# Optimization experiments

Measured on AMD Instinct MI355X. Metric: run time of the kernel, lower is better.

Reference implementation:

```python
import jax, jax.numpy as jnp
import numpy as np
import math

EMBED, HEADS, LEVELS, POINTS = 256, 8, 4, 4
HEAD_DIM = EMBED // HEADS


def _init_offset_bias():
    # replicates MSDeformableAttention._reset_parameters grid init for sampling_offsets.bias
    thetas = np.arange(HEADS, dtype=np.float32) * (2.0 * math.pi / HEADS)
    grid = np.stack([np.cos(thetas), np.sin(thetas)], -1)
    grid = grid / np.abs(grid).max(-1, keepdims=True)
    grid = np.tile(grid.reshape(HEADS, 1, 1, 2), (1, LEVELS, POINTS, 1))
    grid = grid * np.arange(1, POINTS + 1, dtype=np.float32).reshape(1, 1, -1, 1)
    return jnp.asarray(grid.reshape(-1))


def setup_inputs():
    key = jax.random.key(0)
    ks = jax.random.split(key, 8)
    bs, Lq = 4, 900
    shapes = np.array([[100, 100], [50, 50], [25, 25], [13, 13]], dtype=np.int32)
    areas = shapes[:, 0] * shapes[:, 1]
    Lv = int(areas.sum())  # 13294
    start = np.concatenate([[0], np.cumsum(areas)[:-1]]).astype(np.int32)
    s = 0.02
    return {
        'query': jax.random.normal(ks[0], (bs, Lq, EMBED), jnp.float32),
        'reference_points': jax.random.uniform(ks[1], (bs, Lq, LEVELS, 2), jnp.float32),
        'value': jax.random.normal(ks[2], (bs, Lv, EMBED), jnp.float32),
        'value_spatial_shapes': jnp.asarray(shapes),
        'value_level_start_index': jnp.asarray(start),
        'w_value': jax.random.normal(ks[3], (EMBED, EMBED), jnp.float32) * s,
        'b_value': jnp.zeros((EMBED,), jnp.float32),
        'w_offsets': jax.random.normal(ks[4], (HEADS * LEVELS * POINTS * 2, EMBED), jnp.float32) * s,
        'b_offsets': _init_offset_bias(),
        'w_attn': jax.random.normal(ks[5], (HEADS * LEVELS * POINTS, EMBED), jnp.float32) * s,
        'b_attn': jnp.zeros((HEADS * LEVELS * POINTS,), jnp.float32),
        'w_out': jax.random.normal(ks[6], (EMBED, EMBED), jnp.float32) * s,
        'b_out': jnp.zeros((EMBED,), jnp.float32),
    }


def _ms_deform_attn(value, spatial_shapes, start_index, loc, attn):
    # value: [bs, Lv, H, D]; loc: [bs, Lq, H, L, P, 2] normalized in [0,1]; attn: [bs, Lq, H, L, P]
    bs, Lv, nh, hd = value.shape
    Lq = loc.shape[1]
    v = value.transpose(0, 2, 1, 3)  # [bs, H, Lv, D]
    Wf = spatial_shapes[:, 1].astype(loc.dtype).reshape(1, 1, 1, LEVELS, 1)
    Hf = spatial_shapes[:, 0].astype(loc.dtype).reshape(1, 1, 1, LEVELS, 1)
    Wi = spatial_shapes[:, 1].reshape(1, 1, 1, LEVELS, 1)
    Hi = spatial_shapes[:, 0].reshape(1, 1, 1, LEVELS, 1)
    start = start_index.reshape(1, 1, 1, LEVELS, 1)
    # grid_sample(align_corners=False, padding_mode='zeros'): pixel coord = loc * size - 0.5
    x = loc[..., 0] * Wf - 0.5
    y = loc[..., 1] * Hf - 0.5
    x0 = jnp.floor(x)
    y0 = jnp.floor(y)
    lx = x - x0
    ly = y - y0
    x0i = x0.astype(jnp.int32)
    y0i = y0.astype(jnp.int32)

    def corner(xi, yi, w):
        valid = (xi >= 0) & (xi < Wi) & (yi >= 0) & (yi < Hi)
        idx = start + jnp.clip(yi, 0, Hi - 1) * Wi + jnp.clip(xi, 0, Wi - 1)  # global flat index into Lv
        idx = idx.transpose(0, 2, 1, 3, 4).reshape(bs, nh, Lq * LEVELS * POINTS)
        g = jnp.take_along_axis(v, idx[..., None], axis=2)  # [bs, H, Lq*L*P, D]
        g = g.reshape(bs, nh, Lq, LEVELS, POINTS, hd)
        w = (w * valid.astype(loc.dtype)).transpose(0, 2, 1, 3, 4)  # [bs, H, Lq, L, P]
        return g * w[..., None]

    sampled = (corner(x0i, y0i, (1 - lx) * (1 - ly))
               + corner(x0i + 1, y0i, lx * (1 - ly))
               + corner(x0i, y0i + 1, (1 - lx) * ly)
               + corner(x0i + 1, y0i + 1, lx * ly))  # [bs, H, Lq, L, P, D]
    aw = attn.transpose(0, 2, 1, 3, 4)  # [bs, H, Lq, L, P]
    out = (sampled * aw[..., None]).sum(axis=(3, 4))  # [bs, H, Lq, D]
    return out.transpose(0, 2, 1, 3).reshape(bs, Lq, nh * hd)


def reference(query, reference_points, value, value_spatial_shapes, value_level_start_index, w_value, b_value, w_offsets, b_offsets, w_attn, b_attn, w_out, b_out):
    bs, Lq, _ = query.shape
    Lv = value.shape[1]
    v = (value @ w_value.T + b_value).reshape(bs, Lv, HEADS, HEAD_DIM)
    off = (query @ w_offsets.T + b_offsets).reshape(bs, Lq, HEADS, LEVELS, POINTS, 2)
    attn = jax.nn.softmax((query @ w_attn.T + b_attn).reshape(bs, Lq, HEADS, LEVELS * POINTS), axis=-1)
    attn = attn.reshape(bs, Lq, HEADS, LEVELS, POINTS)
    # offset_normalizer = spatial_shapes.flip(1) -> (W, H) per level
    norm = value_spatial_shapes[:, ::-1].astype(query.dtype).reshape(1, 1, 1, LEVELS, 1, 2)
    loc = reference_points[:, :, None, :, None, :] + off / norm  # [bs, Lq, H, L, P, 2]
    out = _ms_deform_attn(v, value_spatial_shapes, value_level_start_index, loc, attn)
    return out @ w_out.T + b_out
```

## Files before the change

kernel.cpp:

```cpp
#include <hip/hip_runtime.h>
#include <cstddef>

#define EMBED 256
#define HEADS 8
#define LEVELS 4
#define POINTS 4
#define NQOUT 384

typedef __attribute__((ext_vector_type(8))) short bf16x8;
typedef __attribute__((ext_vector_type(4))) float f32x4;

__device__ __forceinline__ unsigned short bf16_rn(float x) {
    union { float f; unsigned u; } v; v.f = x;
    const unsigned r = v.u + 0x7fffu + ((v.u >> 16) & 1u);
    return (unsigned short)(r >> 16);
}
__device__ __forceinline__ float bf16_to_f(unsigned short h) {
    union { unsigned u; float f; } v; v.u = (unsigned)h << 16;
    return v.f;
}

__global__ __launch_bounds__(256) void gemm_mfma_split(
    const float* __restrict__ A, const float* __restrict__ B,
    const float* __restrict__ bias, float* __restrict__ C, int M)
{
    __shared__ unsigned short AsH[128 * 32], AsL[128 * 32];
    __shared__ unsigned short BsH[128 * 32], BsL[128 * 32];

    const int tid  = threadIdx.x;
    const int lane = tid & 63;
    const int wid  = tid >> 6;
    const int wm   = (wid >> 1) * 64;
    const int wn   = (wid & 1) * 64;
    const int m0   = blockIdx.y * 128;
    const int n0   = blockIdx.x * 128;

    const int sr = tid >> 1;
    const int sc = (tid & 1) * 16;

    const bool mok = (m0 + sr) < M;
    const float* ga = A + (size_t)(m0 + sr) * 256 + sc;
    const float* gb = B + (size_t)(n0 + sr) * 256 + sc;

    f32x4 acc[4][4] = {};

    for (int k0 = 0; k0 < 256; k0 += 32) {
        #pragma unroll
        for (int i = 0; i < 4; ++i) {
            const int byte_in_row = (sc + i * 4) * 2;
            int addr = sr * 64 + byte_in_row;
            addr ^= (sr & 7) << 4;

            float4 va = make_float4(0.f, 0.f, 0.f, 0.f);
            if (mok) va = *(const float4*)(ga + k0 + i * 4);
            const unsigned short ah0 = bf16_rn(va.x), ah1 = bf16_rn(va.y);
            const unsigned short ah2 = bf16_rn(va.z), ah3 = bf16_rn(va.w);
            const unsigned short al0 = bf16_rn(va.x - bf16_to_f(ah0));
            const unsigned short al1 = bf16_rn(va.y - bf16_to_f(ah1));
            const unsigned short al2 = bf16_rn(va.z - bf16_to_f(ah2));
            const unsigned short al3 = bf16_rn(va.w - bf16_to_f(ah3));
            *(uint2*)((char*)AsH + addr) =
                make_uint2((unsigned)ah0 | ((unsigned)ah1 << 16),
                           (unsigned)ah2 | ((unsigned)ah3 << 16));
            *(uint2*)((char*)AsL + addr) =
                make_uint2((unsigned)al0 | ((unsigned)al1 << 16),
                           (unsigned)al2 | ((unsigned)al3 << 16));

            const float4 vb = *(const float4*)(gb + k0 + i * 4);
            const unsigned short bh0 = bf16_rn(vb.x), bh1 = bf16_rn(vb.y);
            const unsigned short bh2 = bf16_rn(vb.z), bh3 = bf16_rn(vb.w);
            const unsigned short bl0 = bf16_rn(vb.x - bf16_to_f(bh0));
            const unsigned short bl1 = bf16_rn(vb.y - bf16_to_f(bh1));
            const unsigned short bl2 = bf16_rn(vb.z - bf16_to_f(bh2));
            const unsigned short bl3 = bf16_rn(vb.w - bf16_to_f(bh3));
            *(uint2*)((char*)BsH + addr) =
                make_uint2((unsigned)bh0 | ((unsigned)bh1 << 16),
                           (unsigned)bh2 | ((unsigned)bh3 << 16));
            *(uint2*)((char*)BsL + addr) =
                make_uint2((unsigned)bl0 | ((unsigned)bl1 << 16),
                           (unsigned)bl2 | ((unsigned)bl3 << 16));
        }
        __syncthreads();

        bf16x8 ah[4], al[4], bh[4], bl[4];
        const int kb = (lane >> 4) * 16;
        #pragma unroll
        for (int f = 0; f < 4; ++f) {
            const int rowA = wm + f * 16 + (lane & 15);
            int aaddr = rowA * 64 + kb;  aaddr ^= (rowA & 7) << 4;
            ah[f] = *(const bf16x8*)((const char*)AsH + aaddr);
            al[f] = *(const bf16x8*)((const char*)AsL + aaddr);
            const int rowB = wn + f * 16 + (lane & 15);
            int baddr = rowB * 64 + kb;  baddr ^= (rowB & 7) << 4;
            bh[f] = *(const bf16x8*)((const char*)BsH + baddr);
            bl[f] = *(const bf16x8*)((const char*)BsL + baddr);
        }
        #pragma unroll
        for (int mi = 0; mi < 4; ++mi)
            #pragma unroll
            for (int ni = 0; ni < 4; ++ni) {
                acc[mi][ni] = __builtin_amdgcn_mfma_f32_16x16x32_bf16(
                    ah[mi], bh[ni], acc[mi][ni], 0, 0, 0);
                acc[mi][ni] = __builtin_amdgcn_mfma_f32_16x16x32_bf16(
                    ah[mi], bl[ni], acc[mi][ni], 0, 0, 0);
                acc[mi][ni] = __builtin_amdgcn_mfma_f32_16x16x32_bf16(
                    al[mi], bh[ni], acc[mi][ni], 0, 0, 0);
            }
        __syncthreads();
    }

    #pragma unroll
    for (int mi = 0; mi < 4; ++mi) {
        #pragma unroll
        for (int j = 0; j < 4; ++j) {
            const int m = m0 + wm + mi * 16 + ((lane >> 4) << 2) + j;
            if (m >= M) continue;
            #pragma unroll
            for (int ni = 0; ni < 4; ++ni) {
                const int n = n0 + wn + ni * 16 + (lane & 15);
                C[(size_t)m * 256 + n] = acc[mi][ni][j] + bias[n];
            }
        }
    }
}

template<int TM, int TN, int TK>
__global__ __launch_bounds__(256) void gemm_abt_bias(
    const float* __restrict__ A, const float* __restrict__ B,
    const float* __restrict__ bias, float* __restrict__ C,
    int M, int N, int K)
{
    __shared__ float As[TK][TM + 4];
    __shared__ float Bs[TK][TN + 4];
    const int tid = threadIdx.x;
    const int m0 = blockIdx.y * TM;
    const int n0 = blockIdx.x * TN;
    const int tx = tid & 15;
    const int ty = tid >> 4;
    const int ar  = tid >> 2;
    const int ac4 = (tid & 3) << 2;

    float acc[4][4] = {};

    for (int k0 = 0; k0 < K; k0 += TK) {
        {
            const int m = m0 + ar;
            float4 va = make_float4(0.f, 0.f, 0.f, 0.f);
            if (m < M) va = *(const float4*)(A + (size_t)m * K + k0 + ac4);
            As[ac4 + 0][ar] = va.x; As[ac4 + 1][ar] = va.y;
            As[ac4 + 2][ar] = va.z; As[ac4 + 3][ar] = va.w;

            const int n = n0 + ar;
            const float4 vb = *(const float4*)(B + (size_t)n * K + k0 + ac4);
            Bs[ac4 + 0][ar] = vb.x; Bs[ac4 + 1][ar] = vb.y;
            Bs[ac4 + 2][ar] = vb.z; Bs[ac4 + 3][ar] = vb.w;
        }
        __syncthreads();

        #pragma unroll
        for (int k = 0; k < TK; ++k) {
            const float4 a4 = *(const float4*)(&As[k][ty << 2]);
            const float4 b4 = *(const float4*)(&Bs[k][tx << 2]);
            const float a[4] = {a4.x, a4.y, a4.z, a4.w};
            const float b[4] = {b4.x, b4.y, b4.z, b4.w};
            #pragma unroll
            for (int i = 0; i < 4; ++i)
                #pragma unroll
                for (int j = 0; j < 4; ++j)
                    acc[i][j] = fmaf(a[i], b[j], acc[i][j]);
        }
        __syncthreads();
    }

    #pragma unroll
    for (int i = 0; i < 4; ++i) {
        const int m = m0 + (ty << 2) + i;
        if (m >= M) continue;
        #pragma unroll
        for (int j = 0; j < 4; ++j) {
            const int n = n0 + (tx << 2) + j;
            C[(size_t)m * N + n] = acc[i][j] + bias[n];
        }
    }
}

__global__ __launch_bounds__(256) void gemm_query_fused(
    const float* __restrict__ A,
    const float* __restrict__ Boff,  const float* __restrict__ Battn,
    const float* __restrict__ boff,  const float* __restrict__ battn,
    float* __restrict__ C, int M, int K)
{
    constexpr int TM = 64, TN = 64, TK = 16;
    __shared__ float As[TK][TM + 4];
    __shared__ float Bs[TK][TN + 4];
    const int tid = threadIdx.x;
    const int m0 = blockIdx.y * TM;
    const int n0 = blockIdx.x * TN;
    const bool isAttn = (n0 >= 256);
    const float* __restrict__ B  = isAttn ? Battn : Boff;
    const float* __restrict__ bv = isAttn ? battn : boff;
    const int nbase = isAttn ? (n0 - 256) : n0;

    const int tx = tid & 15;
    const int ty = tid >> 4;
    const int ar  = tid >> 2;
    const int ac4 = (tid & 3) << 2;

    float acc[4][4] = {};

    for (int k0 = 0; k0 < K; k0 += TK) {
        {
            const int m = m0 + ar;
            float4 va = make_float4(0.f, 0.f, 0.f, 0.f);
            if (m < M) va = *(const float4*)(A + (size_t)m * K + k0 + ac4);
            As[ac4 + 0][ar] = va.x; As[ac4 + 1][ar] = va.y;
            As[ac4 + 2][ar] = va.z; As[ac4 + 3][ar] = va.w;

            const float4 vb = *(const float4*)(B + (size_t)(nbase + ar) * K + k0 + ac4);
            Bs[ac4 + 0][ar] = vb.x; Bs[ac4 + 1][ar] = vb.y;
            Bs[ac4 + 2][ar] = vb.z; Bs[ac4 + 3][ar] = vb.w;
        }
        __syncthreads();

        #pragma unroll
        for (int k = 0; k < TK; ++k) {
            const float4 a4 = *(const float4*)(&As[k][ty << 2]);
            const float4 b4 = *(const float4*)(&Bs[k][tx << 2]);
            const float a[4] = {a4.x, a4.y, a4.z, a4.w};
            const float b[4] = {b4.x, b4.y, b4.z, b4.w};
            #pragma unroll
            for (int i = 0; i < 4; ++i)
                #pragma unroll
                for (int j = 0; j < 4; ++j)
                    acc[i][j] = fmaf(a[i], b[j], acc[i][j]);
        }
        __syncthreads();
    }

    #pragma unroll
    for (int i = 0; i < 4; ++i) {
        const int m = m0 + (ty << 2) + i;
        if (m >= M) continue;
        #pragma unroll
        for (int j = 0; j < 4; ++j) {
            const int nl = (tx << 2) + j;
            C[(size_t)m * NQOUT + n0 + nl] = acc[i][j] + bv[nbase + nl];
        }
    }
}

__global__ __launch_bounds__(256) void ms_sample_kernel(
    const float* __restrict__ vproj,
    const float* __restrict__ refp,
    const float* __restrict__ qout,
    const int*   __restrict__ shapes,
    const int*   __restrict__ startix,
    float* __restrict__ sampled,
    int Lq, int Lv)
{
    __shared__ float aw_lds[HEADS * LEVELS * POINTS];

    const int bq = blockIdx.x;
    const int b  = bq / Lq;
    const int tid = threadIdx.x;
    const int h = tid >> 5, d = tid & 31;

    const float* vb   = vproj + (size_t)b * Lv * EMBED;
    const float* rowq = qout + (size_t)bq * NQOUT;
    const float* offq = rowq;
    const float* logq = rowq + 256;
    const float* refq = refp + (size_t)bq * LEVELS * 2;

    if (tid < HEADS * LEVELS * POINTS) {
        const float v = logq[tid];
        float m = v;
        #pragma unroll
        for (int s = 8; s > 0; s >>= 1) m = fmaxf(m, __shfl_xor(m, s, 16));
        const float e = __expf(v - m);
        float sum = e;
        #pragma unroll
        for (int s = 8; s > 0; s >>= 1) sum += __shfl_xor(sum, s, 16);
        aw_lds[tid] = e / sum;
    }
    __syncthreads();

    float accv = 0.f;
    #pragma unroll
    for (int l = 0; l < LEVELS; ++l) {
        const int H = shapes[l * 2 + 0];
        const int W = shapes[l * 2 + 1];
        const int st = startix[l];
        const float fW = (float)W, fH = (float)H;
        const float rx = refq[l * 2 + 0];
        const float ry = refq[l * 2 + 1];
        #pragma unroll
        for (int p = 0; p < POINTS; ++p) {
            const int oi = (((h * LEVELS + l) * POINTS) + p) * 2;
            const float ox = offq[oi + 0];
            const float oy = offq[oi + 1];
            const float aw = aw_lds[(h * LEVELS + l) * POINTS + p];
            const float x = (rx + ox / fW) * fW - 0.5f;
            const float y = (ry + oy / fH) * fH - 0.5f;
            const float x0f = floorf(x), y0f = floorf(y);
            const float lx = x - x0f, ly = y - y0f;
            const int x0 = (int)x0f, y0 = (int)y0f;
            float s = 0.f;
            #pragma unroll
            for (int c = 0; c < 4; ++c) {
                const int xi = x0 + (c & 1);
                const int yi = y0 + (c >> 1);
                const float wx = (c & 1) ? lx : 1.f - lx;
                const float wy = (c >> 1) ? ly : 1.f - ly;
                const bool valid = (xi >= 0) && (xi < W) && (yi >= 0) && (yi < H);
                const int xc = min(max(xi, 0), W - 1);
                const int yc = min(max(yi, 0), H - 1);
                const float val = vb[(size_t)(st + yc * W + xc) * EMBED + (h << 5) + d];
                s = fmaf(valid ? wx * wy : 0.f, val, s);
            }
            accv = fmaf(aw, s, accv);
        }
    }
    sampled[(size_t)bq * EMBED + tid] = accv;
}

extern "C" void kernel_launch(void* const* d_in, const int* in_sizes, int n_in,
                              void* d_out, int out_size, void* d_ws, size_t ws_size,
                              hipStream_t stream)
{
    const float* query   = (const float*)d_in[0];
    const float* refp    = (const float*)d_in[1];
    const float* value   = (const float*)d_in[2];
    const int*   shapes  = (const int*)d_in[3];
    const int*   startix = (const int*)d_in[4];
    const float* w_value = (const float*)d_in[5];
    const float* b_value = (const float*)d_in[6];
    const float* w_off   = (const float*)d_in[7];
    const float* b_off   = (const float*)d_in[8];
    const float* w_attn  = (const float*)d_in[9];
    const float* b_attn  = (const float*)d_in[10];
    const float* w_out   = (const float*)d_in[11];
    const float* b_out   = (const float*)d_in[12];
    float* out = (float*)d_out;

    const int bs = 4;
    const int Lq = in_sizes[0] / (bs * EMBED);
    const int Lv = in_sizes[2] / (bs * EMBED);
    const int BQ = bs * Lq;

    float* ws = (float*)d_ws;
    float* vproj   = ws; ws += (size_t)bs * Lv * EMBED;
    float* qoutb   = ws; ws += (size_t)BQ * NQOUT;
    float* sampled = ws; ws += (size_t)BQ * EMBED;

    {
        const int M = bs * Lv;
        dim3 grid(EMBED / 128, (M + 127) / 128);
        hipLaunchKernelGGL(gemm_mfma_split, grid, dim3(256), 0, stream,
                           value, w_value, b_value, vproj, M);
    }
    {
        dim3 grid(NQOUT / 64, (BQ + 63) / 64);
        hipLaunchKernelGGL(gemm_query_fused, grid, dim3(256), 0, stream,
                           query, w_off, w_attn, b_off, b_attn, qoutb, BQ, EMBED);
    }
    {
        hipLaunchKernelGGL(ms_sample_kernel, dim3(BQ), dim3(256), 0, stream,
                           vproj, refp, qoutb, shapes, startix, sampled, Lq, Lv);
    }
    {
        dim3 grid(EMBED / 64, (BQ + 63) / 64);
        hipLaunchKernelGGL((gemm_abt_bias<64, 64, 16>), grid, dim3(256), 0, stream,
                           sampled, w_out, b_out, out, BQ, EMBED, EMBED);
    }
}
```

Baseline: 226.1 us.

## Pre-split value weight into swizzled bf16 hi/lo once and DMA into LDS

Adds a prep kernel that converts w_value into pre-swizzled bf16 hi/lo halves once per call, so the value projection no longer redoes that conversion in every tile. The projection kernel now tiles 64 rows by the full 256 columns, so the A tile is converted only once per row block instead of once per column tile. Weight tiles are loaded straight into LDS with global_load_lds. This costs an extra kernel launch and a larger LDS footprint for B, and there is no double buffering.

Result: no change. 221.7 us (-2.0%).

```diff
diff --git a/kernel.cpp b/kernel.cpp
--- a/kernel.cpp
+++ b/kernel.cpp
@@ -19,66 +19,94 @@
     union { unsigned u; float f; } v; v.u = (unsigned)h << 16;
     return v.f;
 }
-
-__global__ __launch_bounds__(256) void gemm_mfma_split(
-    const float* __restrict__ A, const float* __restrict__ B,
+__device__ __forceinline__ int sw_addr(int row, int byte_in_row) {
+    return (row * 64 + byte_in_row) ^ ((row & 7) << 4);
+}
+
+__global__ __launch_bounds__(256) void prep_w(
+    const float* __restrict__ w,
+    unsigned short* __restrict__ hi, unsigned short* __restrict__ lo)
+{
+    const int t  = blockIdx.x * 256 + threadIdx.x;
+    const int r  = t >> 3;
+    const int kp = t & 7;
+    const float* src = w + (size_t)r * 256 + kp * 32;
+    #pragma unroll
+    for (int c = 0; c < 4; ++c) {
+        unsigned hw[4], lw[4];
+        #pragma unroll
+        for (int j = 0; j < 4; ++j) {
+            const float f0 = src[c * 8 + j * 2 + 0];
+            const float f1 = src[c * 8 + j * 2 + 1];
+            const unsigned short h0 = bf16_rn(f0), h1 = bf16_rn(f1);
+            const unsigned short l0 = bf16_rn(f0 - bf16_to_f(h0));
+            const unsigned short l1 = bf16_rn(f1 - bf16_to_f(h1));
+            hw[j] = (unsigned)h0 | ((unsigned)h1 << 16);
+            lw[j] = (unsigned)l0 | ((unsigned)l1 << 16);
+        }
+        const int addr = kp * 16384 + sw_addr(r, c * 16);
+        *(uint4*)((char*)hi + addr) = make_uint4(hw[0], hw[1], hw[2], hw[3]);
+        *(uint4*)((char*)lo + addr) = make_uint4(lw[0], lw[1], lw[2], lw[3]);
+    }
+}
+
+__global__ __launch_bounds__(256) void vproj_mfma(
+    const float* __restrict__ A,
+    const unsigned short* __restrict__ Bhi, const unsigned short* __restrict__ Blo,
     const float* __restrict__ bias, float* __restrict__ C, int M)
 {
-    __shared__ unsigned short AsH[128 * 32], AsL[128 * 32];
-    __shared__ unsigned short BsH[128 * 32], BsL[128 * 32];
+    __shared__ unsigned short AsH[64 * 32], AsL[64 * 32];
+    __shared__ unsigned short BsH[256 * 32], BsL[256 * 32];
 
     const int tid  = threadIdx.x;
     const int lane = tid & 63;
-    const int wid  = tid >> 6;
-    const int wm   = (wid >> 1) * 64;
-    const int wn   = (wid & 1) * 64;
-    const int m0   = blockIdx.y * 128;
-    const int n0   = blockIdx.x * 128;
-
-    const int sr = tid >> 1;
-    const int sc = (tid & 1) * 16;
-
+    const int wn   = (tid >> 6) * 64;
+    const int m0   = blockIdx.x * 64;
+
+    const int sr = tid >> 2;
+    const int sc = (tid & 3) * 8;
     const bool mok = (m0 + sr) < M;
     const float* ga = A + (size_t)(m0 + sr) * 256 + sc;
-    const float* gb = B + (size_t)(n0 + sr) * 256 + sc;
+
+    const int wbase = (tid & 192) * 16;
 
     f32x4 acc[4][4] = {};
 
-    for (int k0 = 0; k0 < 256; k0 += 32) {
+    for (int kp = 0; kp < 8; ++kp) {
         #pragma unroll
         for (int i = 0; i < 4; ++i) {
-            const int byte_in_row = (sc + i * 4) * 2;
-            int addr = sr * 64 + byte_in_row;
-            addr ^= (sr & 7) << 4;
-
+            const int off = i * 4096 + wbase + (lane << 4);
+            __builtin_amdgcn_global_load_lds(
+                (const __attribute__((address_space(1))) unsigned int*)
+                    ((const char*)Bhi + kp * 16384 + off),
+                (__attribute__((address_space(3))) unsigned int*)
+                    ((char*)BsH + i * 4096 + wbase),
+                16, 0, 0);
+            __builtin_amdgcn_global_load_lds(
+                (const __attribute__((address_space(1))) unsigned int*)
+                    ((const char*)Blo + kp * 16384 + off),
+                (__attribute__((address_space(3))) unsigned int*)
+                    ((char*)BsL + i * 4096 + wbase),
+                16, 0, 0);
+        }
+
+        #pragma unroll
+        for (int q = 0; q < 2; ++q) {
             float4 va = make_float4(0.f, 0.f, 0.f, 0.f);
-            if (mok) va = *(const float4*)(ga + k0 + i * 4);
-            const unsigned short ah0 = bf16_rn(va.x), ah1 = bf16_rn(va.y);
-            const unsigned short ah2 = bf16_rn(va.z), ah3 = bf16_rn(va.w);
-            const unsigned short al0 = bf16_rn(va.x - bf16_to_f(ah0));
-            const unsigned short al1 = bf16_rn(va.y - bf16_to_f(ah1));
-            const unsigned short al2 = bf16_rn(va.z - bf16_to_f(ah2));
-            const unsigned short al3 = bf16_rn(va.w - bf16_to_f(ah3));
+            if (mok) va = *(const float4*)(ga + kp * 32 + q * 4);
+            const unsigned short h0 = bf16_rn(va.x), h1 = bf16_rn(va.y);
+            const unsigned short h2 = bf16_rn(va.z), h3 = bf16_rn(va.w);
+            const unsigned short l0 = bf16_rn(va.x - bf16_to_f(h0));
+            const unsigned short l1 = bf16_rn(va.y - bf16_to_f(h1));
+            const unsigned short l2 = bf16_rn(va.z - bf16_to_f(h2));
+            const unsigned short l3 = bf16_rn(va.w - bf16_to_f(h3));
+            const int addr = sw_addr(sr, (sc + q * 4) * 2);
             *(uint2*)((char*)AsH + addr) =
-                make_uint2((unsigned)ah0 | ((unsigned)ah1 << 16),
-                           (unsigned)ah2 | ((unsigned)ah3 << 16));
+                make_uint2((unsigned)h0 | ((unsigned)h1 << 16),
+                           (unsigned)h2 | ((unsigned)h3 << 16));
             *(uint2*)((char*)AsL + addr) =
-                make_uint2((unsigned)al0 | ((unsigned)al1 << 16),
-                           (unsigned)al2 | ((unsigned)al3 << 16));
-
-            const float4 vb = *(const float4*)(gb + k0 + i * 4);
-            const unsigned short bh0 = bf16_rn(vb.x), bh1 = bf16_rn(vb.y);
-            const unsigned short bh2 = bf16_rn(vb.z), bh3 = bf16_rn(vb.w);
-            const unsigned short bl0 = bf16_rn(vb.x - bf16_to_f(bh0));
-            const unsigned short bl1 = bf16_rn(vb.y - bf16_to_f(bh1));
-            const unsigned short bl2 = bf16_rn(vb.z - bf16_to_f(bh2));
-            const unsigned short bl3 = bf16_rn(vb.w - bf16_to_f(bh3));
-            *(uint2*)((char*)BsH + addr) =
-                make_uint2((unsigned)bh0 | ((unsigned)bh1 << 16),
-                           (unsigned)bh2 | ((unsigned)bh3 << 16));
-            *(uint2*)((char*)BsL + addr) =
-                make_uint2((unsigned)bl0 | ((unsigned)bl1 << 16),
-                           (unsigned)bl2 | ((unsigned)bl3 << 16));
+                make_uint2((unsigned)l0 | ((unsigned)l1 << 16),
+                           (unsigned)l2 | ((unsigned)l3 << 16));
         }
         __syncthreads();
 
@@ -86,12 +114,10 @@
         const int kb = (lane >> 4) * 16;
         #pragma unroll
         for (int f = 0; f < 4; ++f) {
-            const int rowA = wm + f * 16 + (lane & 15);
-            int aaddr = rowA * 64 + kb;  aaddr ^= (rowA & 7) << 4;
+            const int aaddr = sw_addr(f * 16 + (lane & 15), kb);
             ah[f] = *(const bf16x8*)((const char*)AsH + aaddr);
             al[f] = *(const bf16x8*)((const char*)AsL + aaddr);
-            const int rowB = wn + f * 16 + (lane & 15);
-            int baddr = rowB * 64 + kb;  baddr ^= (rowB & 7) << 4;
+            const int baddr = sw_addr(wn + f * 16 + (lane & 15), kb);
             bh[f] = *(const bf16x8*)((const char*)BsH + baddr);
             bl[f] = *(const bf16x8*)((const char*)BsL + baddr);
         }
@@ -113,11 +139,11 @@
     for (int mi = 0; mi < 4; ++mi) {
         #pragma unroll
         for (int j = 0; j < 4; ++j) {
-            const int m = m0 + wm + mi * 16 + ((lane >> 4) << 2) + j;
+            const int m = m0 + mi * 16 + ((lane >> 4) << 2) + j;
             if (m >= M) continue;
             #pragma unroll
             for (int ni = 0; ni < 4; ++ni) {
-                const int n = n0 + wn + ni * 16 + (lane & 15);
+                const int n = wn + ni * 16 + (lane & 15);
                 C[(size_t)m * 256 + n] = acc[mi][ni][j] + bias[n];
             }
         }
@@ -346,27 +372,28 @@
     const int Lq = in_sizes[0] / (bs * EMBED);
     const int Lv = in_sizes[2] / (bs * EMBED);
     const int BQ = bs * Lq;
+    const int M  = bs * Lv;
 
     float* ws = (float*)d_ws;
     float* vproj   = ws; ws += (size_t)bs * Lv * EMBED;
     float* qoutb   = ws; ws += (size_t)BQ * NQOUT;
     float* sampled = ws; ws += (size_t)BQ * EMBED;
-
-    {
-        const int M = bs * Lv;
-        dim3 grid(EMBED / 128, (M + 127) / 128);
-        hipLaunchKernelGGL(gemm_mfma_split, grid, dim3(256), 0, stream,
-                           value, w_value, b_value, vproj, M);
-    }
+    unsigned short* bhi = (unsigned short*)ws;
+    unsigned short* blo = bhi + 256 * 256;
+
+    hipLaunchKernelGGL(prep_w, dim3(8), dim3(256), 0, stream, w_value, bhi, blo);
+
+    hipLaunchKernelGGL(vproj_mfma, dim3((M + 63) / 64), dim3(256), 0, stream,
+                       value, bhi, blo, b_value, vproj, M);
+
     {
         dim3 grid(NQOUT / 64, (BQ + 63) / 64);
         hipLaunchKernelGGL(gemm_query_fused, grid, dim3(256), 0, stream,
                            query, w_off, w_attn, b_off, b_attn, qoutb, BQ, EMBED);
     }
-    {
-        hipLaunchKernelGGL(ms_sample_kernel, dim3(BQ), dim3(256), 0, stream,
-                           vproj, refp, qoutb, shapes, startix, sampled, Lq, Lv);
-    }
+    hipLaunchKernelGGL(ms_sample_kernel, dim3(BQ), dim3(256), 0, stream,
+                       vproj, refp, qoutb, shapes, startix, sampled, Lq, Lv);
+
     {
         dim3 grid(EMBED / 64, (BQ + 63) / 64);
         hipLaunchKernelGGL((gemm_abt_bias<64, 64, 16>), grid, dim3(256), 0, stream,
```
